# Optimization experiments

Measured on AMD Instinct MI355X. Metric: run time of the kernel, lower is better.

The kernel has to match this reference:

```python
import jax, jax.numpy as jnp
import numpy as np

N_PTS = 65536   # input points
M = 4096        # sampled clusters (n_nodes)
K = 16          # knn neighbors
C_IN = 128
C_OUT = 256
BN_EPS = 1e-5


def setup_inputs() -> dict:
    key = jax.random.key(0)
    k1, k2, k3 = jax.random.split(key, 3)
    x = jax.random.normal(k1, (N_PTS, C_IN), jnp.float32)
    pos = jax.random.normal(k2, (N_PTS, 3), jnp.float32)
    batch = jnp.zeros((N_PTS,), jnp.int32)  # single point cloud
    W = jax.random.normal(k3, (C_IN, C_OUT), jnp.float32) / np.sqrt(C_IN)
    b = jnp.zeros((C_OUT,), jnp.float32)
    gamma = jnp.ones((C_OUT,), jnp.float32)
    beta = jnp.zeros((C_OUT,), jnp.float32)
    return {"x": x, "pos": pos, "batch": batch, "W": W, "b": b,
            "gamma": gamma, "beta": beta}


def _fps(pos, m):
    """Farthest point sampling starting from index 0. Returns m indices."""
    n = pos.shape[0]

    def step(carry, _):
        min_d, last = carry
        d = jnp.sum((pos - pos[last]) ** 2, axis=-1)  # [N]
        min_d = jnp.minimum(min_d, d)
        nxt = jnp.argmax(min_d).astype(jnp.int32)
        return (min_d, nxt), nxt

    init = (jnp.full((n,), jnp.inf, pos.dtype), jnp.int32(0))
    _, rest = jax.lax.scan(step, init, None, length=m - 1)
    return jnp.concatenate([jnp.zeros((1,), jnp.int32), rest])


def _knn(pos, sub_pos, k):
    """For each of M query points, indices of k nearest points in pos. [M, k]"""
    # squared euclidean distances, [M, N]
    d2 = (jnp.sum(sub_pos ** 2, -1, keepdims=True)
          - 2.0 * sub_pos @ pos.T
          + jnp.sum(pos ** 2, -1)[None, :])
    _, idx = jax.lax.top_k(-d2, k)
    return idx


def _mlp(x, W, b, gamma, beta):
    # Linear -> BatchNorm1d (training-mode batch stats, biased var) -> ReLU
    h = x @ W + b                      # [N, C_OUT]
    mu = jnp.mean(h, axis=0)
    var = jnp.mean((h - mu) ** 2, axis=0)
    h = gamma * (h - mu) * jax.lax.rsqrt(var + BN_EPS) + beta
    return jax.nn.relu(h)


def reference(x, pos, batch, W, b, gamma, beta):
    id_clusters = _fps(pos, M)                 # [M]
    sub_pos = pos[id_clusters]                 # [M, 3]
    sub_batch = batch[id_clusters]             # [M]
    nbr = _knn(pos, sub_pos, K)                # [M, K]
    h = _mlp(x, W, b, gamma, beta)             # [N, C_OUT]
    # gather + max-pool over each cluster's k neighbors (== scatter_max,
    # since knn emits exactly K neighbors per cluster, grouped by cluster)
    out = jnp.max(h[nbr], axis=1)              # [M, C_OUT]
    return out, sub_pos, sub_batch
```

## Files before the change

kernel.cpp:

```cpp
#include <hip/hip_runtime.h>
#include <hip/hip_bf16.h>

#define N_PTS 65536
#define MCLUS 4096
#define KNN   16
#define C_IN  128
#define C_OUT 256

typedef unsigned long long u64;
typedef unsigned u32;

#define WS_ID     0
#define WS_SLOTS  16384
#define WS_BBOX   49152
#define WS_CNT    49216
#define WS_OFS    180288
#define WS_NBR    49216
#define WS_POS4   311360
#define WS_PSUM   311360
#define WS_PSUMSQ 835648
#define WS_SCALE  1359936
#define WS_SHIFT  1360960

__device__ __forceinline__ u32 fkey(float v) {
    u32 u = __float_as_uint(v);
    return (u >> 31) ? ~u : (u | 0x80000000u);
}
__device__ __forceinline__ float funkey(u32 k) {
    u32 u = (k >> 31) ? (k & 0x7FFFFFFFu) : ~k;
    return __uint_as_float(u);
}

__global__ void init_kernel(int* __restrict__ id, u64* __restrict__ slots,
                            u32* __restrict__ bbox, int* __restrict__ cellcnt) {
    int t = threadIdx.x;
    for (int i = t; i < 4096; i += 1024) slots[i] = 0ull;
    for (int i = t; i < 32768; i += 1024) cellcnt[i] = 0;
    if (t < 3)   bbox[t] = 0xFFFFFFFFu;
    if (t >= 3 && t < 6) bbox[t] = 0u;
    if (t == 0) id[0] = 0;
}

__global__ __launch_bounds__(256) void bbox_kernel(const float* __restrict__ pos,
                                                   u32* __restrict__ bbox) {
    int t = blockIdx.x * 256 + threadIdx.x;
    u32 mn0 = 0xFFFFFFFFu, mn1 = 0xFFFFFFFFu, mn2 = 0xFFFFFFFFu;
    u32 mx0 = 0u, mx1 = 0u, mx2 = 0u;
    for (int i = t; i < N_PTS; i += 16384) {
        u32 k0 = fkey(pos[i*3+0]), k1 = fkey(pos[i*3+1]), k2 = fkey(pos[i*3+2]);
        mn0 = min(mn0, k0); mn1 = min(mn1, k1); mn2 = min(mn2, k2);
        mx0 = max(mx0, k0); mx1 = max(mx1, k1); mx2 = max(mx2, k2);
    }
    #pragma unroll
    for (int off = 32; off > 0; off >>= 1) {
        mn0 = min(mn0, (u32)__shfl_xor(mn0, off)); mx0 = max(mx0, (u32)__shfl_xor(mx0, off));
        mn1 = min(mn1, (u32)__shfl_xor(mn1, off)); mx1 = max(mx1, (u32)__shfl_xor(mx1, off));
        mn2 = min(mn2, (u32)__shfl_xor(mn2, off)); mx2 = max(mx2, (u32)__shfl_xor(mx2, off));
    }
    if ((threadIdx.x & 63) == 0) {
        atomicMin(&bbox[0], mn0); atomicMin(&bbox[1], mn1); atomicMin(&bbox[2], mn2);
        atomicMax(&bbox[3], mx0); atomicMax(&bbox[4], mx1); atomicMax(&bbox[5], mx2);
    }
}

__device__ __forceinline__ int cell_of(float x, float y, float z, const u32* bb) {
    float x0 = funkey(bb[0]), y0 = funkey(bb[1]), z0 = funkey(bb[2]);
    float x1 = funkey(bb[3]), y1 = funkey(bb[4]), z1 = funkey(bb[5]);
    float sx = 32.0f / fmaxf(x1 - x0, 1e-20f);
    float sy = 32.0f / fmaxf(y1 - y0, 1e-20f);
    float sz = 32.0f / fmaxf(z1 - z0, 1e-20f);
    int gx = min(max((int)((x - x0) * sx), 0), 31);
    int gy = min(max((int)((y - y0) * sy), 0), 31);
    int gz = min(max((int)((z - z0) * sz), 0), 31);
    int m = 0;
    #pragma unroll
    for (int k = 0; k < 5; ++k)
        m |= (((gx >> k) & 1) << (3*k + 2)) | (((gy >> k) & 1) << (3*k + 1)) | (((gz >> k) & 1) << (3*k));
    return m;
}

__global__ __launch_bounds__(256) void count_kernel(const float* __restrict__ pos,
                                                    const u32* __restrict__ bbox,
                                                    int* __restrict__ cellcnt) {
    int i = blockIdx.x * 256 + threadIdx.x;
    atomicAdd(&cellcnt[cell_of(pos[i*3+0], pos[i*3+1], pos[i*3+2], bbox)], 1);
}

__global__ __launch_bounds__(1024) void scan_kernel(const int* __restrict__ cellcnt,
                                                    int* __restrict__ cellofs) {
    __shared__ int ts[1024];
    int t = threadIdx.x;
    int v[32]; int s = 0;
    #pragma unroll
    for (int i = 0; i < 32; ++i) { v[i] = cellcnt[t*32 + i]; s += v[i]; }
    ts[t] = s; __syncthreads();
    for (int off = 1; off < 1024; off <<= 1) {
        int u = (t >= off) ? ts[t - off] : 0;
        __syncthreads();
        ts[t] += u;
        __syncthreads();
    }
    int pre = (t == 0) ? 0 : ts[t - 1];
    #pragma unroll
    for (int i = 0; i < 32; ++i) { cellofs[t*32 + i] = pre; pre += v[i]; }
}

__global__ __launch_bounds__(256) void scatter_kernel(const float* __restrict__ pos,
                                                      const u32* __restrict__ bbox,
                                                      int* __restrict__ cellofs,
                                                      float4* __restrict__ pos4) {
    int i = blockIdx.x * 256 + threadIdx.x;
    float x = pos[i*3+0], y = pos[i*3+1], z = pos[i*3+2];
    int o = atomicAdd(&cellofs[cell_of(x, y, z, bbox)], 1);
    pos4[o] = make_float4(x, y, z, __int_as_float(i));
}

__device__ __forceinline__ float dist3(float ax, float ay, float az,
                                       float bx, float by, float bz) {
    float dx = __fsub_rn(ax, bx), dy = __fsub_rn(ay, by), dz = __fsub_rn(az, bz);
    return __fadd_rn(__fadd_rn(__fmul_rn(dx, dx), __fmul_rn(dy, dy)), __fmul_rn(dz, dz));
}

__device__ __forceinline__ u32 wave_max_u32(u32 v) {
    #pragma unroll
    for (int off = 32; off > 0; off >>= 1) {
        u32 o = __shfl_xor(v, off);
        v = o > v ? o : v;
    }
    return v;
}
__device__ __forceinline__ u32 wave_min_u32(u32 v) {
    #pragma unroll
    for (int off = 32; off > 0; off >>= 1) {
        u32 o = __shfl_xor(v, off);
        v = o < v ? o : v;
    }
    return v;
}

__device__ __forceinline__ int wave_argmax48(u64 k48) {
    u32 hi = (u32)(k48 >> 16);
    u32 him = wave_max_u32(hi);
    u64 ball = __ballot(hi == him);
    if (__popcll(ball) > 1) {
        u32 a = (hi == him) ? (u32)(k48 & 0xFFFFull) : 0u;
        u32 am = wave_max_u32(a);
        ball = __ballot((hi == him) && (a == am));
    }
    return __ffsll((long long)ball) - 1;
}

__global__ __launch_bounds__(64) void fps_kernel(const float* __restrict__ pos,
                                                 const float4* __restrict__ pos4,
                                                 int* __restrict__ id,
                                                 u64* __restrict__ slots) {
    const int lane = threadIdx.x;
    const int blk  = blockIdx.x;
    __shared__ float bku[1024];

    float px[16], py[16], pz[16], md[16];
    u32 inv[16];
    const float c0x = pos[0], c0y = pos[1], c0z = pos[2];
    #pragma unroll
    for (int e = 0; e < 16; ++e) {
        int sp = blk * 1024 + (lane >> 3) * 128 + e * 8 + (lane & 7);
        float4 v = pos4[sp];
        px[e] = v.x; py[e] = v.y; pz[e] = v.z;
        inv[e] = 0xFFFFu - (u32)__float_as_int(v.w);
        md[e] = dist3(px[e], py[e], pz[e], c0x, c0y, c0z);
    }

    int r = 0;
    u32 fb_mine = 0xFu;

    auto slow_round = [&](int rr, int s) {
        u64 bk = 0; float bx = 0.f, by = 0.f, bz = 0.f;
        #pragma unroll
        for (int e = 0; e < 16; ++e) {
            u64 k = ((u64)__float_as_uint(md[e]) << 16) | inv[e];
            bool bt = k > bk;
            bk = bt ? k : bk; bx = bt ? px[e] : bx; by = bt ? py[e] : by; bz = bt ? pz[e] : bz;
        }
        int src = wave_argmax48(bk);
        float wx = __shfl(bx, src), wy = __shfl(by, src), wz = __shfl(bz, src);
        u64 kb = __shfl(bk, src);

        const u64 tg = (u64)((rr + 1) & 0xFFFF);
        u64* base = &slots[(u32)(rr & 1) * 2048];
        {
            u64 w0 = (kb << 16) | tg;
            u64 w1 = ((u64)__float_as_uint(wx) << 32) | tg;
            u64 w2 = ((u64)__float_as_uint(wy) << 32) | tg;
            u64 w3 = ((u64)__float_as_uint(wz) << 32) | tg;
            u64 wv = (lane == 0) ? w0 : (lane == 1) ? w1 : (lane == 2) ? w2 : w3;
            if (lane < 4)
                __hip_atomic_store(&base[(u32)blk * 32 + (u32)lane], wv,
                                   __ATOMIC_RELAXED, __HIP_MEMORY_SCOPE_AGENT);
        }
        u64* bp = &base[(u32)lane * 32];
        u64 v0, v1, v2, v3;
        for (;;) {
            v0 = __hip_atomic_load(&bp[0], __ATOMIC_RELAXED, __HIP_MEMORY_SCOPE_AGENT);
            v1 = __hip_atomic_load(&bp[1], __ATOMIC_RELAXED, __HIP_MEMORY_SCOPE_AGENT);
            v2 = __hip_atomic_load(&bp[2], __ATOMIC_RELAXED, __HIP_MEMORY_SCOPE_AGENT);
            v3 = __hip_atomic_load(&bp[3], __ATOMIC_RELAXED, __HIP_MEMORY_SCOPE_AGENT);
            u64 bad = ((v0 ^ tg) | (v1 ^ tg) | (v2 ^ tg) | (v3 ^ tg)) & 0xFFFFull;
            if (bad == 0ull) break;
        }
        u64 k2 = v0 >> 16;
        int s2 = wave_argmax48(k2);
        u64 kw = __shfl(k2, s2);
        float cx = __shfl(__uint_as_float((u32)(v1 >> 32)), s2);
        float cy = __shfl(__uint_as_float((u32)(v2 >> 32)), s2);
        float cz = __shfl(__uint_as_float((u32)(v3 >> 32)), s2);
        if (blk == 0 && lane == 0) id[s] = (int)(0xFFFFu - (u32)(kw & 0xFFFFull));
        #pragma unroll
        for (int e = 0; e < 16; ++e)
            md[e] = fminf(md[e], dist3(px[e], py[e], pz[e], cx, cy, cz));
    };

    u64 wk48[8]; float wxa[8], wya[8], wza[8];

    for (int B = 0; B <= 511; ++B) {
        u64 bk = 0; float bx = 0.f, by = 0.f, bz = 0.f;
        #pragma unroll
        for (int e = 0; e < 16; ++e) {
            u64 k = ((u64)__float_as_uint(md[e]) << 16) | inv[e];
            bool bt = k > bk;
            bk = bt ? k : bk; bx = bt ? px[e] : bx; by = bt ? py[e] : by; bz = bt ? pz[e] : bz;
        }
        u64 ks = bk;
        #pragma unroll
        for (int off = 1; off <= 4; off <<= 1) {
            u64 o = __shfl_xor(ks, off);
            if (o > ks) ks = o;
        }
        {
            u64 ball = __ballot(bk == ks);
            int segbase = (lane >> 3) << 3;
            int ssrc = __ffsll((long long)(ball & (0xFFull << segbase))) - 1;
            bx = __shfl(bx, ssrc); by = __shfl(by, ssrc); bz = __shfl(bz, ssrc);
        }

        const u64 tg = (u64)((r + 1) & 0xFFFF);
        u64* base = &slots[(u32)(r & 1) * 2048];
        {
            int c = lane / 3; if (c > 7) c = 7;
            int p = lane - c * 3;
            int srcl = 8 * c;
            u64 kk  = __shfl(ks, srcl);
            float gx = __shfl(bx, srcl), gy = __shfl(by, srcl), gz = __shfl(bz, srcl);
            u32 hi, mid;
            if (p == 0)      { hi = __float_as_uint(gx); mid = (u32)(kk & 0xFFFFull); }
            else if (p == 1) { hi = __float_as_uint(gy); mid = (u32)(kk >> 32) & 0xFFFFu; }
            else             { hi = __float_as_uint(gz); mid = (u32)(kk >> 16) & 0xFFFFu; }
            u64 wd = ((u64)hi << 32) | ((u64)mid << 16) | tg;
            if (lane == 24) wd = ((u64)(fb_mine & 0xFu) << 16) | tg;
            if (lane < 25)
                __hip_atomic_store(&base[(u32)blk * 32 + (u32)lane], wd,
                                   __ATOMIC_RELAXED, __HIP_MEMORY_SCOPE_AGENT);
        }

        u64 w[25]; u32 valid = 0;
        {
            u64* bp = &base[(u32)lane * 32];
            do {
                #pragma unroll
                for (int i = 0; i < 25; ++i)
                    if (!(valid & (1u << i)))
                        w[i] = __hip_atomic_load(&bp[i], __ATOMIC_RELAXED, __HIP_MEMORY_SCOPE_AGENT);
                #pragma unroll
                for (int i = 0; i < 25; ++i)
                    if ((u32)(w[i] & 0xFFFFull) == (u32)tg) valid |= (1u << i);
            } while (valid != 0x1FFFFFFu);
        }
        ++r;

        u32 jstar = wave_min_u32((u32)(w[24] >> 16) & 0xFu);
        if (jstar < 8u) {
            #pragma unroll
            for (int e = 0; e < 16; ++e) md[e] = bku[e * 64 + lane];
            #pragma unroll
            for (int j = 0; j < 8; ++j) {
                if ((u32)j < jstar) {
                    #pragma unroll
                    for (int e = 0; e < 16; ++e)
                        md[e] = fminf(md[e], dist3(px[e], py[e], pz[e], wxa[j], wya[j], wza[j]));
                }
            }
            int sbase = 8 * (B - 1) + 1;
            for (int sub = (int)jstar; sub < 8; ++sub) { slow_round(r, sbase + sub); ++r; }
            fb_mine = 0xFu;
            --B; continue;
        }
        if (B == 511) break;

        float cpx[8], cpy[8], cpz[8], cmdf[8]; u32 cinv[8];
        #pragma unroll
        for (int c = 0; c < 8; ++c) {
            u64 a = w[3 * c], b = w[3 * c + 1], d = w[3 * c + 2];
            cpx[c] = __uint_as_float((u32)(a >> 32));
            cpy[c] = __uint_as_float((u32)(b >> 32));
            cpz[c] = __uint_as_float((u32)(d >> 32));
            cinv[c] = (u32)(a >> 16) & 0xFFFFu;
            u32 mdb = (((u32)(b >> 16) & 0xFFFFu) << 16) | ((u32)(d >> 16) & 0xFFFFu);
            cmdf[c] = __uint_as_float(mdb);
        }

        float pwx = 0.f, pwy = 0.f, pwz = 0.f;
        #pragma unroll
        for (int j = 0; j < 8; ++j) {
            if (j) {
                #pragma unroll
                for (int c = 0; c < 8; ++c)
                    cmdf[c] = fminf(cmdf[c], dist3(cpx[c], cpy[c], cpz[c], pwx, pwy, pwz));
            }
            u64 bk2 = 0; float b2x = 0.f, b2y = 0.f, b2z = 0.f;
            #pragma unroll
            for (int c = 0; c < 8; ++c) {
                u64 k = ((u64)__float_as_uint(cmdf[c]) << 16) | cinv[c];
                bool bt = k > bk2;
                bk2 = bt ? k : bk2; b2x = bt ? cpx[c] : b2x; b2y = bt ? cpy[c] : b2y; b2z = bt ? cpz[c] : b2z;
            }
            int src = wave_argmax48(bk2);
            u64 kw = __shfl(bk2, src);
            float wx = __shfl(b2x, src), wy = __shfl(b2y, src), wz = __shfl(b2z, src);
            wk48[j] = kw; wxa[j] = wx; wya[j] = wy; wza[j] = wz;
            pwx = wx; pwy = wy; pwz = wz;
            if (blk == 0 && lane == 0) id[8 * B + 1 + j] = (int)(0xFFFFu - (u32)(kw & 0xFFFFull));
        }

        #pragma unroll
        for (int e = 0; e < 16; ++e) bku[e * 64 + lane] = md[e];
        u32 vmask = 0;
        #pragma unroll
        for (int j = 0; j < 8; ++j) {
            #pragma unroll
            for (int e = 0; e < 16; ++e) {
                u64 vk = ((u64)__float_as_uint(md[e]) << 16) | inv[e];
                if (vk > wk48[j]) vmask |= (1u << j);
            }
            #pragma unroll
            for (int e = 0; e < 16; ++e)
                md[e] = fminf(md[e], dist3(px[e], py[e], pz[e], wxa[j], wya[j], wza[j]));
        }
        #pragma unroll
        for (int off = 32; off > 0; off >>= 1) vmask |= (u32)__shfl_xor(vmask, off);
        fb_mine = vmask ? (u32)(__ffs(vmask) - 1) : 0xFu;
    }

    for (int s = 4089; s < 4096; ++s) { slow_round(r, s); ++r; }
}

__global__ void subout_kernel(const float* __restrict__ pos, const int* __restrict__ batch,
                              const int* __restrict__ id, float* __restrict__ sub_pos,
                              int* __restrict__ sub_batch) {
    int m = blockIdx.x * blockDim.x + threadIdx.x;
    if (m >= MCLUS) return;
    int idx = id[m];
    sub_pos[m*3+0] = pos[idx*3+0];
    sub_pos[m*3+1] = pos[idx*3+1];
    sub_pos[m*3+2] = pos[idx*3+2];
    sub_batch[m] = batch[idx];
}

__global__ __launch_bounds__(64) void knn_kernel(const float* __restrict__ pos,
                                                 const int* __restrict__ id,
                                                 int* __restrict__ nbr) {
    const int q = blockIdx.x;
    const int lane = threadIdx.x;
    const int qi = id[q];
    const float qx = pos[qi*3+0], qy = pos[qi*3+1], qz = pos[qi*3+2];
    const float nq = __fadd_rn(__fadd_rn(__fmul_rn(qx,qx), __fmul_rn(qy,qy)), __fmul_rn(qz,qz));

    float dl[KNN]; int il[KNN];
    #pragma unroll
    for (int t = 0; t < KNN; ++t) { dl[t] = __builtin_inff(); il[t] = 0x7FFFFFFF; }

    for (int j = lane; j < N_PTS; j += 64) {
        float px = pos[j*3+0], py = pos[j*3+1], pz = pos[j*3+2];
        float npj = __fadd_rn(__fadd_rn(__fmul_rn(px,px), __fmul_rn(py,py)), __fmul_rn(pz,pz));
        float dot = __fadd_rn(__fadd_rn(__fmul_rn(qx,px), __fmul_rn(qy,py)), __fmul_rn(qz,pz));
        float d2  = __fadd_rn(__fsub_rn(nq, __fmul_rn(2.0f, dot)), npj);
        if (d2 < dl[KNN-1] || (d2 == dl[KNN-1] && j < il[KNN-1])) {
            dl[KNN-1] = d2; il[KNN-1] = j;
            #pragma unroll
            for (int t = KNN-1; t > 0; --t) {
                float a = dl[t-1], bq = dl[t];
                int   ai = il[t-1], bi = il[t];
                bool sw = (bq < a) || (bq == a && bi < ai);
                dl[t-1] = sw ? bq : a;  dl[t] = sw ? a : bq;
                il[t-1] = sw ? bi : ai; il[t] = sw ? ai : bi;
            }
        }
    }

    __shared__ float sd[64][KNN];
    __shared__ int   si[64][KNN];
    #pragma unroll
    for (int t = 0; t < KNN; ++t) { sd[lane][t] = dl[t]; si[lane][t] = il[t]; }
    __syncthreads();

    int ptr = 0;
    for (int rr = 0; rr < KNN; ++rr) {
        unsigned long long key = ~0ull;
        if (ptr < KNN) {
            unsigned u = __float_as_uint(sd[lane][ptr]);
            unsigned mu = (u >> 31) ? ~u : (u | 0x80000000u);
            key = ((unsigned long long)mu << 32) | (unsigned)si[lane][ptr];
        }
        unsigned long long m = key;
        #pragma unroll
        for (int off = 32; off > 0; off >>= 1) {
            unsigned long long o = __shfl_xor(m, off);
            if (o < m) m = o;
        }
        if (key == m) ptr++;
        if (lane == 0) nbr[q*KNN + rr] = (int)(m & 0xFFFFFFFFull);
    }
}

__global__ __launch_bounds__(256) void stats_kernel(const float* __restrict__ x,
                                                    const float* __restrict__ W,
                                                    const float* __restrict__ b,
                                                    float* __restrict__ psum,
                                                    float* __restrict__ psumsq) {
    __shared__ float xl[64*128];
    const int tid = threadIdx.x;
    const int cg = (tid & 63) * 4;
    const int rq = tid >> 6;
    float s0=0,s1=0,s2v=0,s3=0, q0=0,q1=0,q2=0,q3=0;
    const float4 bv = *(const float4*)&b[cg];

    for (int t = 0; t < 2; ++t) {
        const size_t row0 = (size_t)blockIdx.x*128 + (size_t)t*64;
        __syncthreads();
        for (int i = tid*4; i < 64*128; i += 1024)
            *(float4*)&xl[i] = *(const float4*)&x[row0*128 + i];
        __syncthreads();

        float acc[16][4];
        #pragma unroll
        for (int rr = 0; rr < 16; ++rr) { acc[rr][0]=bv.x; acc[rr][1]=bv.y; acc[rr][2]=bv.z; acc[rr][3]=bv.w; }

        for (int k4 = 0; k4 < 32; ++k4) {
            float4 w0 = *(const float4*)&W[(k4*4+0)*256 + cg];
            float4 w1 = *(const float4*)&W[(k4*4+1)*256 + cg];
            float4 w2 = *(const float4*)&W[(k4*4+2)*256 + cg];
            float4 w3 = *(const float4*)&W[(k4*4+3)*256 + cg];
            #pragma unroll
            for (int rr = 0; rr < 16; ++rr) {
                float4 xv = *(float4*)&xl[(rq*16+rr)*128 + k4*4];
                acc[rr][0] = fmaf(xv.w,w3.x, fmaf(xv.z,w2.x, fmaf(xv.y,w1.x, fmaf(xv.x,w0.x, acc[rr][0]))));
                acc[rr][1] = fmaf(xv.w,w3.y, fmaf(xv.z,w2.y, fmaf(xv.y,w1.y, fmaf(xv.x,w0.y, acc[rr][1]))));
                acc[rr][2] = fmaf(xv.w,w3.z, fmaf(xv.z,w2.z, fmaf(xv.y,w1.z, fmaf(xv.x,w0.z, acc[rr][2]))));
                acc[rr][3] = fmaf(xv.w,w3.w, fmaf(xv.z,w2.w, fmaf(xv.y,w1.w, fmaf(xv.x,w0.w, acc[rr][3]))));
            }
        }
        #pragma unroll
        for (int rr = 0; rr < 16; ++rr) {
            s0 += acc[rr][0]; q0 = fmaf(acc[rr][0],acc[rr][0],q0);
            s1 += acc[rr][1]; q1 = fmaf(acc[rr][1],acc[rr][1],q1);
            s2v+= acc[rr][2]; q2 = fmaf(acc[rr][2],acc[rr][2],q2);
            s3 += acc[rr][3]; q3 = fmaf(acc[rr][3],acc[rr][3],q3);
        }
    }
    __syncthreads();
    float* red = xl;
    red[rq*256 + cg+0] = s0; red[rq*256 + cg+1] = s1; red[rq*256 + cg+2] = s2v; red[rq*256 + cg+3] = s3;
    red[1024 + rq*256 + cg+0] = q0; red[1024 + rq*256 + cg+1] = q1;
    red[1024 + rq*256 + cg+2] = q2; red[1024 + rq*256 + cg+3] = q3;
    __syncthreads();
    if (rq == 0) {
        #pragma unroll
        for (int c = 0; c < 4; ++c) {
            int ch = cg + c;
            float ss = red[ch] + red[256+ch] + red[512+ch] + red[768+ch];
            float qq = red[1024+ch] + red[1280+ch] + red[1536+ch] + red[1792+ch];
            psum  [blockIdx.x*256 + ch] = ss;
            psumsq[blockIdx.x*256 + ch] = qq;
        }
    }
}

__global__ void finalize_kernel(const float* __restrict__ psum, const float* __restrict__ psumsq,
                                const float* __restrict__ gamma, const float* __restrict__ beta,
                                float* __restrict__ scale, float* __restrict__ shift) {
    int c = threadIdx.x;
    float s = 0.f, s2 = 0.f;
    for (int bl = 0; bl < 512; ++bl) { s += psum[bl*256+c]; s2 += psumsq[bl*256+c]; }
    float mu  = s  / 65536.0f;
    float var = s2 / 65536.0f - mu*mu;
    float inv = rsqrtf(var + 1e-5f);
    float sc = gamma[c] * inv;
    scale[c] = sc;
    shift[c] = beta[c] - mu * sc;
}

__global__ __launch_bounds__(256) void out_kernel(const float* __restrict__ x,
                                                  const float* __restrict__ W,
                                                  const float* __restrict__ b,
                                                  const int* __restrict__ nbr,
                                                  const float* __restrict__ scale,
                                                  const float* __restrict__ shift,
                                                  float* __restrict__ out) {
    __shared__ float xl[16*128];
    __shared__ int nb[16];
    const int tid = threadIdx.x;
    const int m = blockIdx.x;
    if (tid < 16) nb[tid] = nbr[m*16 + tid];
    __syncthreads();
    for (int i = tid; i < 16*128; i += 256) {
        int rr = i >> 7, k = i & 127;
        xl[i] = x[(size_t)nb[rr]*128 + k];
    }
    __syncthreads();

    float acc[16];
    const float bias = b[tid];
    #pragma unroll
    for (int rr = 0; rr < 16; ++rr) acc[rr] = bias;

    for (int k4 = 0; k4 < 32; ++k4) {
        float w0 = W[(k4*4+0)*256 + tid];
        float w1 = W[(k4*4+1)*256 + tid];
        float w2 = W[(k4*4+2)*256 + tid];
        float w3 = W[(k4*4+3)*256 + tid];
        #pragma unroll
        for (int rr = 0; rr < 16; ++rr) {
            float4 xv = *(float4*)&xl[rr*128 + k4*4];
            acc[rr] = fmaf(xv.w,w3, fmaf(xv.z,w2, fmaf(xv.y,w1, fmaf(xv.x,w0, acc[rr]))));
        }
    }
    const float sc = scale[tid], sh = shift[tid];
    float v = acc[0];
    #pragma unroll
    for (int rr = 1; rr < 16; ++rr) v = (sc >= 0.f) ? fmaxf(v, acc[rr]) : fminf(v, acc[rr]);
    out[(size_t)m*256 + tid] = fmaxf(fmaf(sc, v, sh), 0.f);
}

extern "C" void kernel_launch(void* const* d_in, const int* in_sizes, int n_in,
                              void* d_out, int out_size, void* d_ws, size_t ws_size,
                              hipStream_t stream) {
    const float* x     = (const float*)d_in[0];
    const float* pos   = (const float*)d_in[1];
    const int*   batch = (const int*)  d_in[2];
    const float* W     = (const float*)d_in[3];
    const float* b     = (const float*)d_in[4];
    const float* gamma = (const float*)d_in[5];
    const float* beta  = (const float*)d_in[6];

    float* out      = (float*)d_out;
    float* sub_pos  = out + (size_t)MCLUS*C_OUT;
    int*   sub_batch= (int*)(out + (size_t)MCLUS*C_OUT + (size_t)MCLUS*3);

    char* ws = (char*)d_ws;
    int*    id      = (int*)   (ws + WS_ID);
    u64*    slots   = (u64*)   (ws + WS_SLOTS);
    u32*    bbox    = (u32*)   (ws + WS_BBOX);
    int*    cellcnt = (int*)   (ws + WS_CNT);
    int*    cellofs = (int*)   (ws + WS_OFS);
    int*    nbr     = (int*)   (ws + WS_NBR);
    float4* pos4    = (float4*)(ws + WS_POS4);
    float*  psum    = (float*) (ws + WS_PSUM);
    float*  psumsq  = (float*) (ws + WS_PSUMSQ);
    float*  scalep  = (float*) (ws + WS_SCALE);
    float*  shiftp  = (float*) (ws + WS_SHIFT);

    init_kernel<<<1, 1024, 0, stream>>>(id, slots, bbox, cellcnt);
    bbox_kernel<<<64, 256, 0, stream>>>(pos, bbox);
    count_kernel<<<256, 256, 0, stream>>>(pos, bbox, cellcnt);
    scan_kernel<<<1, 1024, 0, stream>>>(cellcnt, cellofs);
    scatter_kernel<<<256, 256, 0, stream>>>(pos, bbox, cellofs, pos4);
    fps_kernel<<<64, 64, 0, stream>>>(pos, pos4, id, slots);
    subout_kernel<<<16, 256, 0, stream>>>(pos, batch, id, sub_pos, sub_batch);
    knn_kernel<<<MCLUS, 64, 0, stream>>>(pos, id, nbr);
    stats_kernel<<<512, 256, 0, stream>>>(x, W, b, psum, psumsq);
    finalize_kernel<<<1, 256, 0, stream>>>(psum, psumsq, gamma, beta, scalep, shiftp);
    out_kernel<<<MCLUS, 256, 0, stream>>>(x, W, b, nbr, scalep, shiftp, out);
}
```

Before: 7.829 ms.

## Replace brute-force kNN with grid-cell shell search over sorted points

The kNN kernel now reuses the Morton-sorted point grid built for FPS and visits cells in growing cubic shells around each query. Cells whose bounding box cannot beat the current 16th-best distance are pruned, and the search stops early once the shell radius exceeds that bound. This replaces a full scan of all 65536 points per query with a local search. Neighbor indices are stored as 16-bit values, and the workspace layout is shuffled so they fit without overlapping the cell offset array. The cost is more complex per-shell bookkeeping, including prefix scans, binary search and a repeated merge with block syncs.

```diff
diff --git a/kernel.cpp b/kernel.cpp
--- a/kernel.cpp
+++ b/kernel.cpp
@@ -9,18 +9,19 @@
 
 typedef unsigned long long u64;
 typedef unsigned u32;
+typedef unsigned short u16;
 
 #define WS_ID     0
 #define WS_SLOTS  16384
+#define WS_SCALE  16384
+#define WS_SHIFT  17408
 #define WS_BBOX   49152
 #define WS_CNT    49216
+#define WS_NBR    49216
 #define WS_OFS    180288
-#define WS_NBR    49216
 #define WS_POS4   311360
 #define WS_PSUM   311360
 #define WS_PSUMSQ 835648
-#define WS_SCALE  1359936
-#define WS_SHIFT  1360960
 
 __device__ __forceinline__ u32 fkey(float v) {
     u32 u = __float_as_uint(v);
@@ -63,6 +64,14 @@
     }
 }
 
+__device__ __forceinline__ int morton32(int gx, int gy, int gz) {
+    int m = 0;
+    #pragma unroll
+    for (int k = 0; k < 5; ++k)
+        m |= (((gx >> k) & 1) << (3*k + 2)) | (((gy >> k) & 1) << (3*k + 1)) | (((gz >> k) & 1) << (3*k));
+    return m;
+}
+
 __device__ __forceinline__ int cell_of(float x, float y, float z, const u32* bb) {
     float x0 = funkey(bb[0]), y0 = funkey(bb[1]), z0 = funkey(bb[2]);
     float x1 = funkey(bb[3]), y1 = funkey(bb[4]), z1 = funkey(bb[5]);
@@ -72,11 +81,7 @@
     int gx = min(max((int)((x - x0) * sx), 0), 31);
     int gy = min(max((int)((y - y0) * sy), 0), 31);
     int gz = min(max((int)((z - z0) * sz), 0), 31);
-    int m = 0;
-    #pragma unroll
-    for (int k = 0; k < 5; ++k)
-        m |= (((gx >> k) & 1) << (3*k + 2)) | (((gy >> k) & 1) << (3*k + 1)) | (((gz >> k) & 1) << (3*k));
-    return m;
+    return morton32(gx, gy, gz);
 }
 
 __global__ __launch_bounds__(256) void count_kernel(const float* __restrict__ pos,
@@ -365,59 +370,154 @@
 }
 
 __global__ __launch_bounds__(64) void knn_kernel(const float* __restrict__ pos,
+                                                 const float4* __restrict__ pos4,
+                                                 const int* __restrict__ cellend,
+                                                 const u32* __restrict__ bbox,
                                                  const int* __restrict__ id,
-                                                 int* __restrict__ nbr) {
+                                                 u16* __restrict__ nbr) {
     const int q = blockIdx.x;
     const int lane = threadIdx.x;
     const int qi = id[q];
     const float qx = pos[qi*3+0], qy = pos[qi*3+1], qz = pos[qi*3+2];
     const float nq = __fadd_rn(__fadd_rn(__fmul_rn(qx,qx), __fmul_rn(qy,qy)), __fmul_rn(qz,qz));
 
+    const float x0 = funkey(bbox[0]), y0 = funkey(bbox[1]), z0 = funkey(bbox[2]);
+    const float x1 = funkey(bbox[3]), y1 = funkey(bbox[4]), z1 = funkey(bbox[5]);
+    const float sx = 32.0f / fmaxf(x1 - x0, 1e-20f);
+    const float sy = 32.0f / fmaxf(y1 - y0, 1e-20f);
+    const float sz = 32.0f / fmaxf(z1 - z0, 1e-20f);
+    const float wx = (x1 - x0) * 0.03125f, wy = (y1 - y0) * 0.03125f, wz = (z1 - z0) * 0.03125f;
+    const float wmin = fminf(wx, fminf(wy, wz));
+    const int gx = min(max((int)((qx - x0) * sx), 0), 31);
+    const int gy = min(max((int)((qy - y0) * sy), 0), 31);
+    const int gz = min(max((int)((qz - z0) * sz), 0), 31);
+
     float dl[KNN]; int il[KNN];
     #pragma unroll
     for (int t = 0; t < KNN; ++t) { dl[t] = __builtin_inff(); il[t] = 0x7FFFFFFF; }
-
-    for (int j = lane; j < N_PTS; j += 64) {
-        float px = pos[j*3+0], py = pos[j*3+1], pz = pos[j*3+2];
-        float npj = __fadd_rn(__fadd_rn(__fmul_rn(px,px), __fmul_rn(py,py)), __fmul_rn(pz,pz));
-        float dot = __fadd_rn(__fadd_rn(__fmul_rn(qx,px), __fmul_rn(qy,py)), __fmul_rn(qz,pz));
-        float d2  = __fadd_rn(__fsub_rn(nq, __fmul_rn(2.0f, dot)), npj);
-        if (d2 < dl[KNN-1] || (d2 == dl[KNN-1] && j < il[KNN-1])) {
-            dl[KNN-1] = d2; il[KNN-1] = j;
-            #pragma unroll
-            for (int t = KNN-1; t > 0; --t) {
-                float a = dl[t-1], bq = dl[t];
-                int   ai = il[t-1], bi = il[t];
-                bool sw = (bq < a) || (bq == a && bi < ai);
-                dl[t-1] = sw ? bq : a;  dl[t] = sw ? a : bq;
-                il[t-1] = sw ? bi : ai; il[t] = sw ? ai : bi;
-            }
-        }
-    }
 
     __shared__ float sd[64][KNN];
     __shared__ int   si[64][KNN];
-    #pragma unroll
-    for (int t = 0; t < KNN; ++t) { sd[lane][t] = dl[t]; si[lane][t] = il[t]; }
-    __syncthreads();
-
-    int ptr = 0;
-    for (int rr = 0; rr < KNN; ++rr) {
-        unsigned long long key = ~0ull;
-        if (ptr < KNN) {
-            unsigned u = __float_as_uint(sd[lane][ptr]);
-            unsigned mu = (u >> 31) ? ~u : (u | 0x80000000u);
-            key = ((unsigned long long)mu << 32) | (unsigned)si[lane][ptr];
-        }
-        unsigned long long m = key;
-        #pragma unroll
-        for (int off = 32; off > 0; off >>= 1) {
-            unsigned long long o = __shfl_xor(m, off);
-            if (o < m) m = o;
-        }
-        if (key == m) ptr++;
-        if (lane == 0) nbr[q*KNN + rr] = (int)(m & 0xFFFFFFFFull);
-    }
+
+    auto merge16 = [&](bool writeOut) -> float {
+        #pragma unroll
+        for (int t = 0; t < KNN; ++t) { sd[lane][t] = dl[t]; si[lane][t] = il[t]; }
+        __syncthreads();
+        int ptr = 0; u64 m = 0;
+        for (int rr = 0; rr < KNN; ++rr) {
+            u64 key = ~0ull;
+            if (ptr < KNN) {
+                u32 u = __float_as_uint(sd[lane][ptr]);
+                u32 mu = (u >> 31) ? ~u : (u | 0x80000000u);
+                key = ((u64)mu << 32) | (u32)si[lane][ptr];
+            }
+            m = key;
+            #pragma unroll
+            for (int off = 32; off > 0; off >>= 1) {
+                u64 o = __shfl_xor(m, off);
+                if (o < m) m = o;
+            }
+            if (key == m) ptr++;
+            if (writeOut && lane == 0) nbr[q*KNN + rr] = (u16)(m & 0xFFFFull);
+        }
+        __syncthreads();
+        return funkey((u32)(m >> 32));
+    };
+
+    float B = __builtin_inff();
+    for (int R = 0; R < 32; ++R) {
+        const int D = 2*R + 1;
+        const int F = D*D;
+        const int S = (R == 0) ? 1 : (24*R*R + 2);
+        bool any = false;
+        for (int bas = 0; bas < S; bas += 64) {
+            int i = bas + lane;
+            int start = 0, len = 0;
+            if (i < S) {
+                int dx, dy, dz;
+                if (R == 0) { dx = 0; dy = 0; dz = 0; }
+                else if (i < 2*F) {
+                    dz = (i < F) ? -R : R;
+                    int k = (i < F) ? i : i - F;
+                    dx = k % D - R; dy = k / D - R;
+                } else {
+                    int j = i - 2*F, P = 8*R;
+                    dz = -R + 1 + j / P;
+                    int k = j % P;
+                    if (k < D)            { dx = k - R;          dy = -R; }
+                    else if (k < 2*D)     { dx = (k - D) - R;    dy =  R; }
+                    else {
+                        int k3 = k - 2*D;
+                        if (k3 < 2*R - 1) { dx = -R; dy = k3 - R + 1; }
+                        else              { dx =  R; dy = (k3 - (2*R - 1)) - R + 1; }
+                    }
+                }
+                int cx = gx + dx, cy = gy + dy, cz = gz + dz;
+                if ((u32)cx < 32u && (u32)cy < 32u && (u32)cz < 32u) {
+                    float lx = (cx == 0)  ? -3.4e38f : x0 + (float)cx * wx;
+                    float hx = (cx == 31) ?  3.4e38f : x0 + (float)(cx+1) * wx;
+                    float ly = (cy == 0)  ? -3.4e38f : y0 + (float)cy * wy;
+                    float hy = (cy == 31) ?  3.4e38f : y0 + (float)(cy+1) * wy;
+                    float lz = (cz == 0)  ? -3.4e38f : z0 + (float)cz * wz;
+                    float hz = (cz == 31) ?  3.4e38f : z0 + (float)(cz+1) * wz;
+                    float ddx = fmaxf(fmaxf(lx - qx, qx - hx), 0.f);
+                    float ddy = fmaxf(fmaxf(ly - qy, qy - hy), 0.f);
+                    float ddz = fmaxf(fmaxf(lz - qz, qz - hz), 0.f);
+                    float md2 = ddx*ddx + ddy*ddy + ddz*ddz;
+                    if (md2 * 0.999f - 1e-3f <= B) {
+                        int mc = morton32(cx, cy, cz);
+                        int end = cellend[mc];
+                        start = mc ? cellend[mc-1] : 0;
+                        len = end - start;
+                    }
+                }
+            }
+            u32 pre = (u32)len;
+            #pragma unroll
+            for (int off = 1; off < 64; off <<= 1) {
+                u32 o = __shfl_up(pre, off);
+                if (lane >= off) pre += o;
+            }
+            u32 T = __shfl(pre, 63);
+            pre -= (u32)len;
+            if (T == 0) continue;
+            any = true;
+            u32 Tpad = (T + 63u) & ~63u;
+            for (u32 t = (u32)lane; t < Tpad; t += 64) {
+                bool act = (t < T);
+                u32 tt = act ? t : (T - 1u);
+                int s = 0;
+                #pragma unroll
+                for (int step = 32; step > 0; step >>= 1) {
+                    int c = s + step;
+                    u32 pc = (u32)__shfl(pre, c);
+                    if (pc <= tt) s = c;
+                }
+                u32 p0 = (u32)__shfl(pre, s);
+                int st = __shfl(start, s);
+                float4 pt = pos4[st + (int)(tt - p0)];
+                float npj = __fadd_rn(__fadd_rn(__fmul_rn(pt.x,pt.x), __fmul_rn(pt.y,pt.y)), __fmul_rn(pt.z,pt.z));
+                float dot = __fadd_rn(__fadd_rn(__fmul_rn(qx,pt.x), __fmul_rn(qy,pt.y)), __fmul_rn(qz,pt.z));
+                float d2  = __fadd_rn(__fsub_rn(nq, __fmul_rn(2.0f, dot)), npj);
+                int oi = __float_as_int(pt.w);
+                if (act && (d2 < dl[KNN-1] || (d2 == dl[KNN-1] && oi < il[KNN-1]))) {
+                    dl[KNN-1] = d2; il[KNN-1] = oi;
+                    #pragma unroll
+                    for (int t2 = KNN-1; t2 > 0; --t2) {
+                        float a = dl[t2-1], bq = dl[t2];
+                        int   ai = il[t2-1], bi = il[t2];
+                        bool sw = (bq < a) || (bq == a && bi < ai);
+                        dl[t2-1] = sw ? bq : a;  dl[t2] = sw ? a : bq;
+                        il[t2-1] = sw ? bi : ai; il[t2] = sw ? ai : bi;
+                    }
+                }
+            }
+        }
+        if (any) B = merge16(false);
+        float rw = (float)R * wmin;
+        if (rw * rw * 0.999f - 1e-3f > B) break;
+    }
+    merge16(true);
 }
 
 __global__ __launch_bounds__(256) void stats_kernel(const float* __restrict__ x,
@@ -500,7 +600,7 @@
 __global__ __launch_bounds__(256) void out_kernel(const float* __restrict__ x,
                                                   const float* __restrict__ W,
                                                   const float* __restrict__ b,
-                                                  const int* __restrict__ nbr,
+                                                  const u16* __restrict__ nbr,
                                                   const float* __restrict__ scale,
                                                   const float* __restrict__ shift,
                                                   float* __restrict__ out) {
@@ -508,7 +608,7 @@
     __shared__ int nb[16];
     const int tid = threadIdx.x;
     const int m = blockIdx.x;
-    if (tid < 16) nb[tid] = nbr[m*16 + tid];
+    if (tid < 16) nb[tid] = (int)nbr[m*16 + tid];
     __syncthreads();
     for (int i = tid; i < 16*128; i += 256) {
         int rr = i >> 7, k = i & 127;
@@ -557,15 +657,15 @@
     char* ws = (char*)d_ws;
     int*    id      = (int*)   (ws + WS_ID);
     u64*    slots   = (u64*)   (ws + WS_SLOTS);
+    float*  scalep  = (float*) (ws + WS_SCALE);
+    float*  shiftp  = (float*) (ws + WS_SHIFT);
     u32*    bbox    = (u32*)   (ws + WS_BBOX);
     int*    cellcnt = (int*)   (ws + WS_CNT);
+    u16*    nbr     = (u16*)   (ws + WS_NBR);
     int*    cellofs = (int*)   (ws + WS_OFS);
-    int*    nbr     = (int*)   (ws + WS_NBR);
     float4* pos4    = (float4*)(ws + WS_POS4);
     float*  psum    = (float*) (ws + WS_PSUM);
     float*  psumsq  = (float*) (ws + WS_PSUMSQ);
-    float*  scalep  = (float*) (ws + WS_SCALE);
-    float*  shiftp  = (float*) (ws + WS_SHIFT);
 
     init_kernel<<<1, 1024, 0, stream>>>(id, slots, bbox, cellcnt);
     bbox_kernel<<<64, 256, 0, stream>>>(pos, bbox);
@@ -574,7 +674,7 @@
     scatter_kernel<<<256, 256, 0, stream>>>(pos, bbox, cellofs, pos4);
     fps_kernel<<<64, 64, 0, stream>>>(pos, pos4, id, slots);
     subout_kernel<<<16, 256, 0, stream>>>(pos, batch, id, sub_pos, sub_batch);
-    knn_kernel<<<MCLUS, 64, 0, stream>>>(pos, id, nbr);
+    knn_kernel<<<MCLUS, 64, 0, stream>>>(pos, pos4, cellofs, bbox, id, nbr);
     stats_kernel<<<512, 256, 0, stream>>>(x, W, b, psum, psumsq);
     finalize_kernel<<<1, 256, 0, stream>>>(psum, psumsq, gamma, beta, scalep, shiftp);
     out_kernel<<<MCLUS, 256, 0, stream>>>(x, W, b, nbr, scalep, shiftp, out);
```

Measured after the change: 6.703 ms (median of 2 runs). 1.17x faster.
